# Performance work log

Measured on AMD Instinct MI355X. Metric: run time of the kernel, lower is better.

Reference implementation:

```python
import jax, jax.numpy as jnp
import numpy as np


def setup_inputs() -> dict:
    key = jax.random.key(0)
    k1, k2 = jax.random.split(key)
    B, C, H, W_ = 16, 512, 64, 64
    x = jax.random.normal(k1, (B, C, H, W_), dtype=jnp.float32)
    W = jax.random.normal(k2, (C, C), dtype=jnp.float32) * (1.0 / np.sqrt(C))
    return {"x": x, "W": W}


def reference(x, W):
    B, C, H, Wd = x.shape
    hw = H * Wd
    x1 = x.reshape(B, C, hw)                      # [B, C, HW]
    # linearW applied to x1^T: [B, HW, C] @ W^T -> [B, HW, C]
    x1_corr = jnp.einsum('bch,dc->bhd', x1, W)    # [B, HW, C]
    s = jnp.einsum('bch,bhd->bcd', x1, x1_corr)   # [B, C, C]
    a = jax.nn.softmax(s, axis=2)
    a = jax.nn.softmax(a, axis=1)
    out = jnp.einsum('bcd,bdh->bch', a, x1) + x1  # [B, C, HW]
    return out.reshape(B, C, H, Wd)
```

## Files before the change

### kernel.cpp

```cpp
#include <hip/hip_runtime.h>


typedef __attribute__((ext_vector_type(8))) short bf16x8;
typedef __attribute__((ext_vector_type(4))) float f32x4;

#define DEVINL __device__ __forceinline__
#define CFENCE() asm volatile("" ::: "memory")

DEVINL unsigned short f2bf(float f) {
  union { float f; unsigned int u; } c; c.f = f;
  unsigned int u = c.u;
  u += 0x7fffu + ((u >> 16) & 1u);
  return (unsigned short)(u >> 16);
}

DEVINL float bf2f(unsigned short h) {
  union { unsigned int u; float f; } c; c.u = ((unsigned int)h) << 16;
  return c.f;
}

DEVINL void gld_lds16(const unsigned short* g, unsigned short* l) {
  __builtin_amdgcn_global_load_lds(
      (const __attribute__((address_space(1))) unsigned int*)g,
      (__attribute__((address_space(3))) unsigned int*)l,
      16 , 0, 0);
}

template<int N> DEVINL void vm_wait() {
  if constexpr (N == 0)       asm volatile("s_waitcnt vmcnt(0)" ::: "memory");
  else if constexpr (N == 2)  asm volatile("s_waitcnt vmcnt(2)" ::: "memory");
  else if constexpr (N == 4)  asm volatile("s_waitcnt vmcnt(4)" ::: "memory");
  else if constexpr (N == 6)  asm volatile("s_waitcnt vmcnt(6)" ::: "memory");
  else if constexpr (N == 8)  asm volatile("s_waitcnt vmcnt(8)" ::: "memory");
  else if constexpr (N == 12) asm volatile("s_waitcnt vmcnt(12)" ::: "memory");
  else static_assert(N < 0, "unsupported vmcnt");
}

DEVINL void sym_tile_decode(int t, int& tm, int& tn) {
  if (t < 4)      { tm = 0; tn = t; }
  else if (t < 7) { tm = 1; tn = t - 3; }
  else if (t < 9) { tm = 2; tn = t - 5; }
  else            { tm = 3; tn = 3; }
}

__global__ __launch_bounds__(256)
void cvt_kernel(const float* __restrict__ in, unsigned short* __restrict__ out, int n4) {
  int i = blockIdx.x * 256 + threadIdx.x;
  const int stride = gridDim.x * 256;
  for (; i < n4; i += stride) {
    float4 v = ((const float4*)in)[i];
    unsigned int lo = (unsigned int)f2bf(v.x) | ((unsigned int)f2bf(v.y) << 16);
    unsigned int hi = (unsigned int)f2bf(v.z) | ((unsigned int)f2bf(v.w) << 16);
    uint2 o; o.x = lo; o.y = hi;
    ((uint2*)out)[i] = o;
  }
}

__global__ __launch_bounds__(256)
void fused_cvt_transpose(const float* __restrict__ x, unsigned short* __restrict__ x_bf,
                         unsigned short* __restrict__ xT) {
  __shared__ unsigned int T[2][32][68];
  const int tid = threadIdx.x;
  const int b  = blockIdx.y;
  const int hs = blockIdx.x & 31;
  const int ct = blockIdx.x >> 5;
  const int h0 = hs * 128;
  const int hq = tid & 7;
  const int c2 = tid >> 3;

  uint4 pa[2], pb[2];
  long long rowA[2];
  #pragma unroll
  for (int hh = 0; hh < 2; ++hh) {
    const int hcol = h0 + hh * 64 + hq * 8;
    rowA[hh] = (long long)(b * 512 + ct * 64 + 2 * c2) * 4096 + hcol;
    float4 a0 = *(const float4*)(x + rowA[hh]);
    float4 a1 = *(const float4*)(x + rowA[hh] + 4);
    float4 b0 = *(const float4*)(x + rowA[hh] + 4096);
    float4 b1 = *(const float4*)(x + rowA[hh] + 4100);
    unsigned short ha[8], hb[8];
    ha[0]=f2bf(a0.x); ha[1]=f2bf(a0.y); ha[2]=f2bf(a0.z); ha[3]=f2bf(a0.w);
    ha[4]=f2bf(a1.x); ha[5]=f2bf(a1.y); ha[6]=f2bf(a1.z); ha[7]=f2bf(a1.w);
    hb[0]=f2bf(b0.x); hb[1]=f2bf(b0.y); hb[2]=f2bf(b0.z); hb[3]=f2bf(b0.w);
    hb[4]=f2bf(b1.x); hb[5]=f2bf(b1.y); hb[6]=f2bf(b1.z); hb[7]=f2bf(b1.w);
    pa[hh].x = (unsigned int)ha[0] | ((unsigned int)ha[1] << 16);
    pa[hh].y = (unsigned int)ha[2] | ((unsigned int)ha[3] << 16);
    pa[hh].z = (unsigned int)ha[4] | ((unsigned int)ha[5] << 16);
    pa[hh].w = (unsigned int)ha[6] | ((unsigned int)ha[7] << 16);
    pb[hh].x = (unsigned int)hb[0] | ((unsigned int)hb[1] << 16);
    pb[hh].y = (unsigned int)hb[2] | ((unsigned int)hb[3] << 16);
    pb[hh].z = (unsigned int)hb[4] | ((unsigned int)hb[5] << 16);
    pb[hh].w = (unsigned int)hb[6] | ((unsigned int)hb[7] << 16);
    uint4 u0, u1;
    u0.x = (unsigned int)ha[0] | ((unsigned int)hb[0] << 16);
    u0.y = (unsigned int)ha[1] | ((unsigned int)hb[1] << 16);
    u0.z = (unsigned int)ha[2] | ((unsigned int)hb[2] << 16);
    u0.w = (unsigned int)ha[3] | ((unsigned int)hb[3] << 16);
    u1.x = (unsigned int)ha[4] | ((unsigned int)hb[4] << 16);
    u1.y = (unsigned int)ha[5] | ((unsigned int)hb[5] << 16);
    u1.z = (unsigned int)ha[6] | ((unsigned int)hb[6] << 16);
    u1.w = (unsigned int)ha[7] | ((unsigned int)hb[7] << 16);
    *(uint4*)&T[hh][c2][hq * 8]     = u0;
    *(uint4*)&T[hh][c2][hq * 8 + 4] = u1;
  }
  asm volatile("s_waitcnt lgkmcnt(0)" ::: "memory");
  __builtin_amdgcn_s_barrier();
  #pragma unroll
  for (int hh = 0; hh < 2; ++hh) {
    *(uint4*)(x_bf + rowA[hh])        = pa[hh];
    *(uint4*)(x_bf + rowA[hh] + 4096) = pb[hh];
  }
  const int h = tid >> 2, seg = tid & 3;
  #pragma unroll
  for (int hh = 0; hh < 2; ++hh) {
    unsigned int uu[8];
    #pragma unroll
    for (int i = 0; i < 8; ++i) uu[i] = T[hh][seg * 8 + i][h];
    unsigned int* dst = (unsigned int*)(xT +
        ((long long)(b * 4096 + h0 + hh * 64 + h) * 512 + ct * 64 + seg * 16));
    uint4 o0, o1;
    o0.x = uu[0]; o0.y = uu[1]; o0.z = uu[2]; o0.w = uu[3];
    o1.x = uu[4]; o1.y = uu[5]; o1.z = uu[6]; o1.w = uu[7];
    *(uint4*)dst = o0;
    *((uint4*)dst + 1) = o1;
  }
}

__global__ __launch_bounds__(256)
void gemm_gsym(const unsigned short* __restrict__ X, float* __restrict__ P) {
  constexpr int HALF = 128 * 32;
  __shared__ unsigned short As[3 * HALF];
  __shared__ unsigned short Bs[3 * HALF];
  const int tid = threadIdx.x;
  const int l   = tid & 63;
  const int w   = tid >> 6;
  const int wr  = w >> 1, wc = w & 1;
  const int b   = blockIdx.y;
  const int t   = blockIdx.x >> 2;
  const int split = blockIdx.x & 3;
  int tm, tn; sym_tile_decode(t, tm, tn);

  const unsigned short* Ab = X + (long long)b * 2097152 + (long long)(tm * 128) * 4096;
  const unsigned short* Bb = X + (long long)b * 2097152 + (long long)(tn * 128) * 4096;

  f32x4 acc[4][4];
  #pragma unroll
  for (int m = 0; m < 4; ++m)
    #pragma unroll
    for (int n = 0; n < 4; ++n) acc[m][n] = (f32x4){0.f, 0.f, 0.f, 0.f};

  const int srow = tid >> 2;
  const int scol = ((tid & 3) ^ ((tid >> 3) & 3)) * 8;
  const int ch8  = (((l >> 4) ^ ((l >> 1) & 3)) * 8);

  auto stage = [&](int buf, int k0) {
    #pragma unroll
    for (int i = 0; i < 2; ++i)
      gld_lds16(Ab + (long long)(i * 64 + srow) * 4096 + k0 + scol, &As[buf * HALF + i * 2048 + tid * 8]);
    #pragma unroll
    for (int i = 0; i < 2; ++i)
      gld_lds16(Bb + (long long)(i * 64 + srow) * 4096 + k0 + scol, &Bs[buf * HALF + i * 2048 + tid * 8]);
  };
  auto compute = [&](int buf) {
    bf16x8 af[4], bfr[4];
    #pragma unroll
    for (int m = 0; m < 4; ++m)
      af[m] = *(const bf16x8*)&As[buf * HALF + (wr * 64 + m * 16 + (l & 15)) * 32 + ch8];
    #pragma unroll
    for (int n = 0; n < 4; ++n)
      bfr[n] = *(const bf16x8*)&Bs[buf * HALF + (wc * 64 + n * 16 + (l & 15)) * 32 + ch8];
    __builtin_amdgcn_s_setprio(1);
    #pragma unroll
    for (int m = 0; m < 4; ++m)
      #pragma unroll
      for (int n = 0; n < 4; ++n)
        acc[m][n] = __builtin_amdgcn_mfma_f32_16x16x32_bf16(af[m], bfr[n], acc[m][n], 0, 0, 0);
    __builtin_amdgcn_s_setprio(0);
  };

  const int k_beg = split * 1024;
  constexpr int NK = 32;
  stage(0, k_beg);
  stage(1, k_beg + 32);
  int cb = 0, sbuf = 2, ks = k_beg + 64;
  for (int k = 0; k < NK - 2; ++k) {
    stage(sbuf, ks);
    ks += 32;
    sbuf = (sbuf == 2) ? 0 : sbuf + 1;
    vm_wait<8>();
    CFENCE(); __builtin_amdgcn_s_barrier(); CFENCE();
    compute(cb);
    CFENCE(); __builtin_amdgcn_s_barrier(); CFENCE();
    cb = (cb == 2) ? 0 : cb + 1;
  }
  vm_wait<4>();
  CFENCE(); __builtin_amdgcn_s_barrier(); CFENCE();
  compute(cb);
  cb = (cb == 2) ? 0 : cb + 1;
  vm_wait<0>();
  CFENCE(); __builtin_amdgcn_s_barrier(); CFENCE();
  compute(cb);

  float* Pt = P + (((long long)b * 10 + t) * 4 + split) * 16384;
  const int cc = l & 15, r4 = (l >> 4) * 4;
  #pragma unroll
  for (int m = 0; m < 4; ++m) {
    #pragma unroll
    for (int n = 0; n < 4; ++n) {
      const int row = wr * 64 + m * 16 + r4;
      const int col = wc * 64 + n * 16 + cc;
      #pragma unroll
      for (int j = 0; j < 4; ++j)
        Pt[(row + j) * 128 + col] = acc[m][n][j];
    }
  }
}

__global__ __launch_bounds__(256)
void reduce_mirror(const float* __restrict__ P, unsigned short* __restrict__ G) {
  __shared__ unsigned short T[128 * 129];
  const int tid = threadIdx.x;
  const int b = blockIdx.y;
  const int t = blockIdx.x;
  int tm, tn; sym_tile_decode(t, tm, tn);
  const float* Pt = P + ((long long)(b * 10 + t) * 4) * 16384;
  unsigned short* Gb = G + (long long)b * 262144;

  #pragma unroll
  for (int e = 0; e < 16; ++e) {
    const int v = e * 256 + tid;
    float4 s0 = ((const float4*)Pt)[v];
    float4 s1 = ((const float4*)(Pt + 16384))[v];
    float4 s2 = ((const float4*)(Pt + 32768))[v];
    float4 s3 = ((const float4*)(Pt + 49152))[v];
    unsigned int h0 = f2bf(s0.x + s1.x + s2.x + s3.x);
    unsigned int h1 = f2bf(s0.y + s1.y + s2.y + s3.y);
    unsigned int h2 = f2bf(s0.z + s1.z + s2.z + s3.z);
    unsigned int h3 = f2bf(s0.w + s1.w + s2.w + s3.w);
    const int idx = v * 4;
    const int r = idx >> 7, c = idx & 127;
    unsigned int* gp = (unsigned int*)(Gb + (long long)(tm * 128 + r) * 512 + tn * 128 + c);
    gp[0] = h0 | (h1 << 16);
    gp[1] = h2 | (h3 << 16);
    unsigned short* tp = &T[r * 129 + c];
    tp[0] = (unsigned short)h0; tp[1] = (unsigned short)h1;
    tp[2] = (unsigned short)h2; tp[3] = (unsigned short)h3;
  }
  if (tm != tn) {
    __syncthreads();
    #pragma unroll
    for (int e = 0; e < 16; ++e) {
      const int idx = (e * 256 + tid) * 4;
      const int r = idx >> 7, c = idx & 127;
      unsigned int o0 = T[(c + 0) * 129 + r], o1 = T[(c + 1) * 129 + r];
      unsigned int o2 = T[(c + 2) * 129 + r], o3 = T[(c + 3) * 129 + r];
      unsigned int* gp = (unsigned int*)(Gb + (long long)(tn * 128 + r) * 512 + tm * 128 + c);
      gp[0] = o0 | (o1 << 16);
      gp[1] = o2 | (o3 << 16);
    }
  }
}

__global__ __launch_bounds__(256)
void gemm_s(const unsigned short* __restrict__ A, const unsigned short* __restrict__ B,
            float* __restrict__ C) {
  constexpr int HALF = 64 * 32;
  __shared__ unsigned short As[3 * HALF];
  __shared__ unsigned short Bs[3 * HALF];

  const int tid = threadIdx.x;
  const int l   = tid & 63;
  const int w   = tid >> 6;
  const int wr  = w >> 1, wc = w & 1;
  const int bz  = blockIdx.y;
  const int tm  = blockIdx.x >> 3;
  const int tn  = blockIdx.x & 7;

  const unsigned short* Ab = A + (long long)bz * 262144 + (long long)(tm * 64) * 512;
  const unsigned short* Bb = B + (long long)(tn * 64) * 512;

  f32x4 acc[2][2];
  #pragma unroll
  for (int m = 0; m < 2; ++m)
    #pragma unroll
    for (int n = 0; n < 2; ++n) acc[m][n] = (f32x4){0.f, 0.f, 0.f, 0.f};

  const int srow = tid >> 2;
  const int scol = ((tid & 3) ^ ((tid >> 3) & 3)) * 8;
  const int ch8  = (((l >> 4) ^ ((l >> 1) & 3)) * 8);

  auto stage = [&](int buf, int k0) {
    gld_lds16(Ab + (long long)srow * 512 + k0 + scol, &As[buf * HALF + tid * 8]);
    gld_lds16(Bb + (long long)srow * 512 + k0 + scol, &Bs[buf * HALF + tid * 8]);
  };
  auto compute = [&](int buf) {
    bf16x8 af[2], bfr[2];
    #pragma unroll
    for (int m = 0; m < 2; ++m)
      af[m] = *(const bf16x8*)&As[buf * HALF + (wr * 32 + m * 16 + (l & 15)) * 32 + ch8];
    #pragma unroll
    for (int n = 0; n < 2; ++n)
      bfr[n] = *(const bf16x8*)&Bs[buf * HALF + (wc * 32 + n * 16 + (l & 15)) * 32 + ch8];
    __builtin_amdgcn_s_setprio(1);
    #pragma unroll
    for (int m = 0; m < 2; ++m)
      #pragma unroll
      for (int n = 0; n < 2; ++n)
        acc[m][n] = __builtin_amdgcn_mfma_f32_16x16x32_bf16(af[m], bfr[n], acc[m][n], 0, 0, 0);
    __builtin_amdgcn_s_setprio(0);
  };

  stage(0, 0);
  stage(1, 32);
  int cb = 0, sbuf = 2, ks = 64;
  for (int k = 0; k < 14; ++k) {
    stage(sbuf, ks);
    ks += 32;
    sbuf = (sbuf == 2) ? 0 : sbuf + 1;
    vm_wait<4>();
    CFENCE(); __builtin_amdgcn_s_barrier(); CFENCE();
    compute(cb);
    CFENCE(); __builtin_amdgcn_s_barrier(); CFENCE();
    cb = (cb == 2) ? 0 : cb + 1;
  }
  vm_wait<2>();
  CFENCE(); __builtin_amdgcn_s_barrier(); CFENCE();
  compute(cb);
  cb = (cb == 2) ? 0 : cb + 1;
  vm_wait<0>();
  CFENCE(); __builtin_amdgcn_s_barrier(); CFENCE();
  compute(cb);

  const int cc = l & 15, r4 = (l >> 4) * 4;
  const int row0 = tm * 64 + wr * 32;
  const int col0 = tn * 64 + wc * 32;
  #pragma unroll
  for (int m = 0; m < 2; ++m) {
    #pragma unroll
    for (int n = 0; n < 2; ++n) {
      const int row = row0 + m * 16 + r4;
      const int col = col0 + n * 16 + cc;
      long long base = (long long)bz * 262144 + (long long)row * 512 + col;
      #pragma unroll
      for (int j = 0; j < 4; ++j)
        C[base + (long long)j * 512] = acc[m][n][j];
    }
  }
}

__global__ __launch_bounds__(256)
void gemm_out(const unsigned short* __restrict__ A, const unsigned short* __restrict__ B,
              float* __restrict__ C) {
  constexpr int HALF_A = 128 * 32;
  constexpr int HALF_B = 256 * 32;
  __shared__ unsigned short As[3 * HALF_A];
  __shared__ unsigned short Bs[3 * HALF_B];

  const int tid = threadIdx.x;
  const int l   = tid & 63;
  const int w   = tid >> 6;
  const int bz  = blockIdx.y;
  const int tm  = blockIdx.x >> 4;
  const int tn  = blockIdx.x & 15;

  const unsigned short* Ab = A + (long long)bz * 262144  + (long long)(tm * 128) * 512;
  const unsigned short* Bb = B + (long long)bz * 2097152 + (long long)(tn * 256) * 512;

  f32x4 acc[8][4];
  #pragma unroll
  for (int m = 0; m < 8; ++m)
    #pragma unroll
    for (int n = 0; n < 4; ++n) acc[m][n] = (f32x4){0.f, 0.f, 0.f, 0.f};

  const int srow = tid >> 2;
  const int scol = ((tid & 3) ^ ((tid >> 3) & 3)) * 8;
  const int ch8  = (((l >> 4) ^ ((l >> 1) & 3)) * 8);

  auto stage = [&](int buf, int k0) {
    #pragma unroll
    for (int i = 0; i < 2; ++i)
      gld_lds16(Ab + (long long)(i * 64 + srow) * 512 + k0 + scol, &As[buf * HALF_A + i * 2048 + tid * 8]);
    #pragma unroll
    for (int i = 0; i < 4; ++i)
      gld_lds16(Bb + (long long)(i * 64 + srow) * 512 + k0 + scol, &Bs[buf * HALF_B + i * 2048 + tid * 8]);
  };
  auto compute = [&](int buf) {
    bf16x8 af[8], bfr[4];
    #pragma unroll
    for (int m = 0; m < 8; ++m)
      af[m] = *(const bf16x8*)&As[buf * HALF_A + (m * 16 + (l & 15)) * 32 + ch8];
    #pragma unroll
    for (int n = 0; n < 4; ++n)
      bfr[n] = *(const bf16x8*)&Bs[buf * HALF_B + (w * 64 + n * 16 + (l & 15)) * 32 + ch8];
    __builtin_amdgcn_s_setprio(1);
    #pragma unroll
    for (int m = 0; m < 8; ++m)
      #pragma unroll
      for (int n = 0; n < 4; ++n)
        acc[m][n] = __builtin_amdgcn_mfma_f32_16x16x32_bf16(af[m], bfr[n], acc[m][n], 0, 0, 0);
    __builtin_amdgcn_s_setprio(0);
  };

  stage(0, 0);
  stage(1, 32);
  int cb = 0, sbuf = 2, ks = 64;
  for (int k = 0; k < 14; ++k) {
    stage(sbuf, ks);
    ks += 32;
    sbuf = (sbuf == 2) ? 0 : sbuf + 1;
    vm_wait<12>();
    CFENCE(); __builtin_amdgcn_s_barrier(); CFENCE();
    compute(cb);
    CFENCE(); __builtin_amdgcn_s_barrier(); CFENCE();
    cb = (cb == 2) ? 0 : cb + 1;
  }
  vm_wait<6>();
  CFENCE(); __builtin_amdgcn_s_barrier(); CFENCE();
  compute(cb);
  cb = (cb == 2) ? 0 : cb + 1;
  vm_wait<0>();
  CFENCE(); __builtin_amdgcn_s_barrier(); CFENCE();
  compute(cb);

  const int cc = l & 15, r4 = (l >> 4) * 4;
  const int row0 = tm * 128;
  const int col0 = tn * 256 + w * 64;
  #pragma unroll
  for (int m = 0; m < 8; ++m) {
    #pragma unroll
    for (int n = 0; n < 4; ++n) {
      const int row = row0 + m * 16 + r4;
      const int col = col0 + n * 16 + cc;
      long long base = (long long)bz * 2097152 + (long long)row * 4096 + col;
      #pragma unroll
      for (int j = 0; j < 4; ++j)
        C[base + (long long)j * 4096] = acc[m][n][j];
    }
  }
}

__global__ __launch_bounds__(256)
void row_softmax_kernel(const float* __restrict__ s, unsigned short* __restrict__ p_bf) {
  __shared__ float red[4], red2[4];
  const float* p = s + (long long)blockIdx.x * 512;
  unsigned short* q = p_bf + (long long)blockIdx.x * 512;
  const int tid = threadIdx.x;
  float v0 = p[tid], v1 = p[tid + 256];
  float m = fmaxf(v0, v1);
  #pragma unroll
  for (int i = 1; i < 64; i <<= 1) m = fmaxf(m, __shfl_xor(m, i));
  if ((tid & 63) == 0) red[tid >> 6] = m;
  __syncthreads();
  m = fmaxf(fmaxf(red[0], red[1]), fmaxf(red[2], red[3]));
  float e0 = __expf(v0 - m), e1 = __expf(v1 - m);
  float sum = e0 + e1;
  #pragma unroll
  for (int i = 1; i < 64; i <<= 1) sum += __shfl_xor(sum, i);
  if ((tid & 63) == 0) red2[tid >> 6] = sum;
  __syncthreads();
  sum = (red2[0] + red2[1]) + (red2[2] + red2[3]);
  float inv = 1.0f / sum;
  q[tid] = f2bf(e0 * inv);
  q[tid + 256] = f2bf(e1 * inv);
}

__global__ __launch_bounds__(256)
void col_softmax_kernel(const unsigned short* __restrict__ p_bf, unsigned short* __restrict__ a_bf) {
  __shared__ float cs[8][32];
  const int tid = threadIdx.x;
  const int dl = tid & 31;
  const int st = tid >> 5;
  const int d  = blockIdx.x * 32 + dl;
  const long long base = (long long)blockIdx.y * 262144 + d;
  const unsigned short* p = p_bf + base;
  float sum = 0.f;
  #pragma unroll 4
  for (int c = st * 64; c < st * 64 + 64; ++c)
    sum += __expf(bf2f(p[(long long)c * 512]));
  cs[st][dl] = sum;
  __syncthreads();
  if (st == 0) {
    float s = ((cs[0][dl] + cs[1][dl]) + (cs[2][dl] + cs[3][dl]))
            + ((cs[4][dl] + cs[5][dl]) + (cs[6][dl] + cs[7][dl]));
    cs[0][dl] = 1.0f / s;
  }
  __syncthreads();
  const float inv = cs[0][dl];
  unsigned short* q = a_bf + base;
  #pragma unroll 4
  for (int c = st * 64; c < st * 64 + 64; ++c) {
    float v = __expf(bf2f(p[(long long)c * 512])) * inv;
    if (c == d) v += 1.0f;
    q[(long long)c * 512] = f2bf(v);
  }
}

extern "C" void kernel_launch(void* const* d_in, const int* in_sizes, int n_in,
                              void* d_out, int out_size, void* d_ws, size_t ws_size,
                              hipStream_t stream) {
  (void)in_sizes; (void)n_in; (void)out_size; (void)ws_size;
  const float* x = (const float*)d_in[0];
  const float* W = (const float*)d_in[1];
  float* out = (float*)d_out;
  char* ws = (char*)d_ws;

  unsigned short* x_bf = (unsigned short*)d_out;
  float* P = (float*)((char*)d_out + 67108864);
  unsigned short* p_bf = (unsigned short*)((char*)d_out + 67108864);

  unsigned short* xT   = (unsigned short*)ws;
  unsigned short* G_bf = (unsigned short*)(ws + 67108864);
  float*          s_f  = (float*)(ws + 75497472);
  unsigned short* W_bf = (unsigned short*)(ws + 92274688);
  unsigned short* a_bf = G_bf;

  fused_cvt_transpose<<<dim3(256, 16), 256, 0, stream>>>(x, x_bf, xT);
  cvt_kernel<<<256, 256, 0, stream>>>(W, W_bf, 65536);

  gemm_gsym<<<dim3(40, 16), 256, 0, stream>>>(x_bf, P);

  reduce_mirror<<<dim3(10, 16), 256, 0, stream>>>(P, G_bf);

  gemm_s<<<dim3(64, 16), 256, 0, stream>>>(G_bf, W_bf, s_f);

  row_softmax_kernel<<<8192, 256, 0, stream>>>(s_f, p_bf);
  col_softmax_kernel<<<dim3(16, 16), 256, 0, stream>>>(p_bf, a_bf);

  gemm_out<<<dim3(64, 16), 256, 0, stream>>>(a_bf, xT, out);
}
```

Measured before the change: 189.0 us.

## Drop xT transpose, transpose X in gemm_out LDS, bf16 split-K partials

Removes the fused convert+transpose kernel and its extra write of a transposed bf16 copy of x. gemm_out now reads row-major x_bf directly, interleaving pairs of rows in registers before writing them to padded LDS, with a new double-buffered pipeline and a 128x128 tile on twice as many blocks. The split-K partials from gemm_gsym are stored as bf16 instead of fp32, halving that traffic at some precision cost. Pipelines in gemm_gsym and gemm_s drop from triple to double buffering, and output stores become nontemporal.

```diff
diff --git a/kernel.cpp b/kernel.cpp
--- a/kernel.cpp
+++ b/kernel.cpp
@@ -32,9 +32,10 @@
   else if constexpr (N == 4)  asm volatile("s_waitcnt vmcnt(4)" ::: "memory");
   else if constexpr (N == 6)  asm volatile("s_waitcnt vmcnt(6)" ::: "memory");
   else if constexpr (N == 8)  asm volatile("s_waitcnt vmcnt(8)" ::: "memory");
-  else if constexpr (N == 12) asm volatile("s_waitcnt vmcnt(12)" ::: "memory");
   else static_assert(N < 0, "unsupported vmcnt");
 }
+
+DEVINL void lgkm0() { asm volatile("s_waitcnt lgkmcnt(0)" ::: "memory"); }
 
 DEVINL void sym_tile_decode(int t, int& tm, int& tn) {
   if (t < 4)      { tm = 0; tn = t; }
@@ -57,80 +58,10 @@
 }
 
 __global__ __launch_bounds__(256)
-void fused_cvt_transpose(const float* __restrict__ x, unsigned short* __restrict__ x_bf,
-                         unsigned short* __restrict__ xT) {
-  __shared__ unsigned int T[2][32][68];
-  const int tid = threadIdx.x;
-  const int b  = blockIdx.y;
-  const int hs = blockIdx.x & 31;
-  const int ct = blockIdx.x >> 5;
-  const int h0 = hs * 128;
-  const int hq = tid & 7;
-  const int c2 = tid >> 3;
-
-  uint4 pa[2], pb[2];
-  long long rowA[2];
-  #pragma unroll
-  for (int hh = 0; hh < 2; ++hh) {
-    const int hcol = h0 + hh * 64 + hq * 8;
-    rowA[hh] = (long long)(b * 512 + ct * 64 + 2 * c2) * 4096 + hcol;
-    float4 a0 = *(const float4*)(x + rowA[hh]);
-    float4 a1 = *(const float4*)(x + rowA[hh] + 4);
-    float4 b0 = *(const float4*)(x + rowA[hh] + 4096);
-    float4 b1 = *(const float4*)(x + rowA[hh] + 4100);
-    unsigned short ha[8], hb[8];
-    ha[0]=f2bf(a0.x); ha[1]=f2bf(a0.y); ha[2]=f2bf(a0.z); ha[3]=f2bf(a0.w);
-    ha[4]=f2bf(a1.x); ha[5]=f2bf(a1.y); ha[6]=f2bf(a1.z); ha[7]=f2bf(a1.w);
-    hb[0]=f2bf(b0.x); hb[1]=f2bf(b0.y); hb[2]=f2bf(b0.z); hb[3]=f2bf(b0.w);
-    hb[4]=f2bf(b1.x); hb[5]=f2bf(b1.y); hb[6]=f2bf(b1.z); hb[7]=f2bf(b1.w);
-    pa[hh].x = (unsigned int)ha[0] | ((unsigned int)ha[1] << 16);
-    pa[hh].y = (unsigned int)ha[2] | ((unsigned int)ha[3] << 16);
-    pa[hh].z = (unsigned int)ha[4] | ((unsigned int)ha[5] << 16);
-    pa[hh].w = (unsigned int)ha[6] | ((unsigned int)ha[7] << 16);
-    pb[hh].x = (unsigned int)hb[0] | ((unsigned int)hb[1] << 16);
-    pb[hh].y = (unsigned int)hb[2] | ((unsigned int)hb[3] << 16);
-    pb[hh].z = (unsigned int)hb[4] | ((unsigned int)hb[5] << 16);
-    pb[hh].w = (unsigned int)hb[6] | ((unsigned int)hb[7] << 16);
-    uint4 u0, u1;
-    u0.x = (unsigned int)ha[0] | ((unsigned int)hb[0] << 16);
-    u0.y = (unsigned int)ha[1] | ((unsigned int)hb[1] << 16);
-    u0.z = (unsigned int)ha[2] | ((unsigned int)hb[2] << 16);
-    u0.w = (unsigned int)ha[3] | ((unsigned int)hb[3] << 16);
-    u1.x = (unsigned int)ha[4] | ((unsigned int)hb[4] << 16);
-    u1.y = (unsigned int)ha[5] | ((unsigned int)hb[5] << 16);
-    u1.z = (unsigned int)ha[6] | ((unsigned int)hb[6] << 16);
-    u1.w = (unsigned int)ha[7] | ((unsigned int)hb[7] << 16);
-    *(uint4*)&T[hh][c2][hq * 8]     = u0;
-    *(uint4*)&T[hh][c2][hq * 8 + 4] = u1;
-  }
-  asm volatile("s_waitcnt lgkmcnt(0)" ::: "memory");
-  __builtin_amdgcn_s_barrier();
-  #pragma unroll
-  for (int hh = 0; hh < 2; ++hh) {
-    *(uint4*)(x_bf + rowA[hh])        = pa[hh];
-    *(uint4*)(x_bf + rowA[hh] + 4096) = pb[hh];
-  }
-  const int h = tid >> 2, seg = tid & 3;
-  #pragma unroll
-  for (int hh = 0; hh < 2; ++hh) {
-    unsigned int uu[8];
-    #pragma unroll
-    for (int i = 0; i < 8; ++i) uu[i] = T[hh][seg * 8 + i][h];
-    unsigned int* dst = (unsigned int*)(xT +
-        ((long long)(b * 4096 + h0 + hh * 64 + h) * 512 + ct * 64 + seg * 16));
-    uint4 o0, o1;
-    o0.x = uu[0]; o0.y = uu[1]; o0.z = uu[2]; o0.w = uu[3];
-    o1.x = uu[4]; o1.y = uu[5]; o1.z = uu[6]; o1.w = uu[7];
-    *(uint4*)dst = o0;
-    *((uint4*)dst + 1) = o1;
-  }
-}
-
-__global__ __launch_bounds__(256)
-void gemm_gsym(const unsigned short* __restrict__ X, float* __restrict__ P) {
+void gemm_gsym(const unsigned short* __restrict__ X, unsigned short* __restrict__ P) {
   constexpr int HALF = 128 * 32;
-  __shared__ unsigned short As[3 * HALF];
-  __shared__ unsigned short Bs[3 * HALF];
+  __shared__ unsigned short As[2 * HALF];
+  __shared__ unsigned short Bs[2 * HALF];
   const int tid = threadIdx.x;
   const int l   = tid & 63;
   const int w   = tid >> 6;
@@ -182,26 +113,22 @@
   constexpr int NK = 32;
   stage(0, k_beg);
   stage(1, k_beg + 32);
-  int cb = 0, sbuf = 2, ks = k_beg + 64;
+  int ks = k_beg + 64;
   for (int k = 0; k < NK - 2; ++k) {
-    stage(sbuf, ks);
-    ks += 32;
-    sbuf = (sbuf == 2) ? 0 : sbuf + 1;
-    vm_wait<8>();
-    CFENCE(); __builtin_amdgcn_s_barrier(); CFENCE();
-    compute(cb);
-    CFENCE(); __builtin_amdgcn_s_barrier(); CFENCE();
-    cb = (cb == 2) ? 0 : cb + 1;
+    vm_wait<4>();
+    CFENCE(); __builtin_amdgcn_s_barrier(); CFENCE();
+    compute(k & 1);
+    CFENCE(); __builtin_amdgcn_s_barrier(); CFENCE();
+    stage(k & 1, ks); ks += 32;
   }
   vm_wait<4>();
   CFENCE(); __builtin_amdgcn_s_barrier(); CFENCE();
-  compute(cb);
-  cb = (cb == 2) ? 0 : cb + 1;
+  compute((NK - 2) & 1);
   vm_wait<0>();
   CFENCE(); __builtin_amdgcn_s_barrier(); CFENCE();
-  compute(cb);
-
-  float* Pt = P + (((long long)b * 10 + t) * 4 + split) * 16384;
+  compute((NK - 1) & 1);
+
+  unsigned short* Pt = P + (((long long)b * 10 + t) * 4 + split) * 16384;
   const int cc = l & 15, r4 = (l >> 4) * 4;
   #pragma unroll
   for (int m = 0; m < 4; ++m) {
@@ -211,32 +138,32 @@
       const int col = wc * 64 + n * 16 + cc;
       #pragma unroll
       for (int j = 0; j < 4; ++j)
-        Pt[(row + j) * 128 + col] = acc[m][n][j];
+        Pt[(row + j) * 128 + col] = f2bf(acc[m][n][j]);
     }
   }
 }
 
 __global__ __launch_bounds__(256)
-void reduce_mirror(const float* __restrict__ P, unsigned short* __restrict__ G) {
+void reduce_mirror(const unsigned short* __restrict__ P, unsigned short* __restrict__ G) {
   __shared__ unsigned short T[128 * 129];
   const int tid = threadIdx.x;
   const int b = blockIdx.y;
   const int t = blockIdx.x;
   int tm, tn; sym_tile_decode(t, tm, tn);
-  const float* Pt = P + ((long long)(b * 10 + t) * 4) * 16384;
+  const unsigned short* Pt = P + ((long long)(b * 10 + t) * 4) * 16384;
   unsigned short* Gb = G + (long long)b * 262144;
 
   #pragma unroll
   for (int e = 0; e < 16; ++e) {
     const int v = e * 256 + tid;
-    float4 s0 = ((const float4*)Pt)[v];
-    float4 s1 = ((const float4*)(Pt + 16384))[v];
-    float4 s2 = ((const float4*)(Pt + 32768))[v];
-    float4 s3 = ((const float4*)(Pt + 49152))[v];
-    unsigned int h0 = f2bf(s0.x + s1.x + s2.x + s3.x);
-    unsigned int h1 = f2bf(s0.y + s1.y + s2.y + s3.y);
-    unsigned int h2 = f2bf(s0.z + s1.z + s2.z + s3.z);
-    unsigned int h3 = f2bf(s0.w + s1.w + s2.w + s3.w);
+    ushort4 s0 = ((const ushort4*)Pt)[v];
+    ushort4 s1 = ((const ushort4*)(Pt + 16384))[v];
+    ushort4 s2 = ((const ushort4*)(Pt + 32768))[v];
+    ushort4 s3 = ((const ushort4*)(Pt + 49152))[v];
+    unsigned int h0 = f2bf(bf2f(s0.x) + bf2f(s1.x) + bf2f(s2.x) + bf2f(s3.x));
+    unsigned int h1 = f2bf(bf2f(s0.y) + bf2f(s1.y) + bf2f(s2.y) + bf2f(s3.y));
+    unsigned int h2 = f2bf(bf2f(s0.z) + bf2f(s1.z) + bf2f(s2.z) + bf2f(s3.z));
+    unsigned int h3 = f2bf(bf2f(s0.w) + bf2f(s1.w) + bf2f(s2.w) + bf2f(s3.w));
     const int idx = v * 4;
     const int r = idx >> 7, c = idx & 127;
     unsigned int* gp = (unsigned int*)(Gb + (long long)(tm * 128 + r) * 512 + tn * 128 + c);
@@ -265,8 +192,8 @@
 void gemm_s(const unsigned short* __restrict__ A, const unsigned short* __restrict__ B,
             float* __restrict__ C) {
   constexpr int HALF = 64 * 32;
-  __shared__ unsigned short As[3 * HALF];
-  __shared__ unsigned short Bs[3 * HALF];
+  __shared__ unsigned short As[2 * HALF];
+  __shared__ unsigned short Bs[2 * HALF];
 
   const int tid = threadIdx.x;
   const int l   = tid & 63;
@@ -312,24 +239,20 @@
 
   stage(0, 0);
   stage(1, 32);
-  int cb = 0, sbuf = 2, ks = 64;
+  int ks = 64;
   for (int k = 0; k < 14; ++k) {
-    stage(sbuf, ks);
-    ks += 32;
-    sbuf = (sbuf == 2) ? 0 : sbuf + 1;
-    vm_wait<4>();
-    CFENCE(); __builtin_amdgcn_s_barrier(); CFENCE();
-    compute(cb);
-    CFENCE(); __builtin_amdgcn_s_barrier(); CFENCE();
-    cb = (cb == 2) ? 0 : cb + 1;
+    vm_wait<2>();
+    CFENCE(); __builtin_amdgcn_s_barrier(); CFENCE();
+    compute(k & 1);
+    CFENCE(); __builtin_amdgcn_s_barrier(); CFENCE();
+    stage(k & 1, ks); ks += 32;
   }
   vm_wait<2>();
   CFENCE(); __builtin_amdgcn_s_barrier(); CFENCE();
-  compute(cb);
-  cb = (cb == 2) ? 0 : cb + 1;
+  compute(0);
   vm_wait<0>();
   CFENCE(); __builtin_amdgcn_s_barrier(); CFENCE();
-  compute(cb);
+  compute(1);
 
   const int cc = l & 15, r4 = (l >> 4) * 4;
   const int row0 = tm * 64 + wr * 32;
@@ -349,84 +272,125 @@
 }
 
 __global__ __launch_bounds__(256)
-void gemm_out(const unsigned short* __restrict__ A, const unsigned short* __restrict__ B,
+void gemm_out(const unsigned short* __restrict__ A, const unsigned short* __restrict__ X,
               float* __restrict__ C) {
-  constexpr int HALF_A = 128 * 32;
-  constexpr int HALF_B = 256 * 32;
-  __shared__ unsigned short As[3 * HALF_A];
-  __shared__ unsigned short Bs[3 * HALF_B];
+  __shared__ unsigned short As[2][128 * 32];
+  __shared__ unsigned int   Bs[2][16][132];
 
   const int tid = threadIdx.x;
   const int l   = tid & 63;
   const int w   = tid >> 6;
+  const int wr  = w >> 1, wc = w & 1;
   const int bz  = blockIdx.y;
-  const int tm  = blockIdx.x >> 4;
-  const int tn  = blockIdx.x & 15;
+  const int tm  = blockIdx.x >> 5;
+  const int tn  = blockIdx.x & 31;
 
   const unsigned short* Ab = A + (long long)bz * 262144  + (long long)(tm * 128) * 512;
-  const unsigned short* Bb = B + (long long)bz * 2097152 + (long long)(tn * 256) * 512;
-
-  f32x4 acc[8][4];
-  #pragma unroll
-  for (int m = 0; m < 8; ++m)
+  const unsigned short* Xb = X + (long long)bz * 2097152 + tn * 128;
+
+  f32x4 acc[4][4];
+  #pragma unroll
+  for (int m = 0; m < 4; ++m)
     #pragma unroll
     for (int n = 0; n < 4; ++n) acc[m][n] = (f32x4){0.f, 0.f, 0.f, 0.f};
 
   const int srow = tid >> 2;
   const int scol = ((tid & 3) ^ ((tid >> 3) & 3)) * 8;
   const int ch8  = (((l >> 4) ^ ((l >> 1) & 3)) * 8);
-
-  auto stage = [&](int buf, int k0) {
+  const int bp_  = tid >> 4;
+  const int bh_  = tid & 15;
+  const unsigned short* Bsrc = Xb + (long long)(2 * bp_) * 4096 + bh_ * 8;
+
+  auto Agload = [&](int buf, int k0) {
     #pragma unroll
     for (int i = 0; i < 2; ++i)
-      gld_lds16(Ab + (long long)(i * 64 + srow) * 512 + k0 + scol, &As[buf * HALF_A + i * 2048 + tid * 8]);
-    #pragma unroll
-    for (int i = 0; i < 4; ++i)
-      gld_lds16(Bb + (long long)(i * 64 + srow) * 512 + k0 + scol, &Bs[buf * HALF_B + i * 2048 + tid * 8]);
+      gld_lds16(Ab + (long long)(i * 64 + srow) * 512 + k0 + scol, &As[buf][i * 2048 + tid * 8]);
+  };
+  auto Bload = [&](int k0, uint4& g0, uint4& g1) {
+    g0 = *(const uint4*)(Bsrc + (long long)k0 * 4096);
+    g1 = *(const uint4*)(Bsrc + (long long)(k0 + 1) * 4096);
+  };
+  auto Bdswrite = [&](int buf, const uint4& g0, const uint4& g1) {
+    unsigned int w0 = (g0.x & 0xffffu) | (g1.x << 16);
+    unsigned int w1 = (g0.x >> 16)    | (g1.x & 0xffff0000u);
+    unsigned int w2 = (g0.y & 0xffffu) | (g1.y << 16);
+    unsigned int w3 = (g0.y >> 16)    | (g1.y & 0xffff0000u);
+    unsigned int w4 = (g0.z & 0xffffu) | (g1.z << 16);
+    unsigned int w5 = (g0.z >> 16)    | (g1.z & 0xffff0000u);
+    unsigned int w6 = (g0.w & 0xffffu) | (g1.w << 16);
+    unsigned int w7 = (g0.w >> 16)    | (g1.w & 0xffff0000u);
+    unsigned int* dst = &Bs[buf][bp_][bh_ * 8];
+    uint4 o0; o0.x = w0; o0.y = w1; o0.z = w2; o0.w = w3;
+    uint4 o1; o1.x = w4; o1.y = w5; o1.z = w6; o1.w = w7;
+    *(uint4*)dst = o0;
+    *(uint4*)(dst + 4) = o1;
   };
   auto compute = [&](int buf) {
-    bf16x8 af[8], bfr[4];
-    #pragma unroll
-    for (int m = 0; m < 8; ++m)
-      af[m] = *(const bf16x8*)&As[buf * HALF_A + (m * 16 + (l & 15)) * 32 + ch8];
-    #pragma unroll
-    for (int n = 0; n < 4; ++n)
-      bfr[n] = *(const bf16x8*)&Bs[buf * HALF_B + (w * 64 + n * 16 + (l & 15)) * 32 + ch8];
+    bf16x8 af[4], bfr[4];
+    #pragma unroll
+    for (int m = 0; m < 4; ++m)
+      af[m] = *(const bf16x8*)&As[buf][(wr * 64 + m * 16 + (l & 15)) * 32 + ch8];
+    const int hl = wc * 64 + (l & 15);
+    const int p0 = (l >> 4) * 4;
+    #pragma unroll
+    for (int n = 0; n < 4; ++n) {
+      unsigned int wv[4];
+      #pragma unroll
+      for (int i = 0; i < 4; ++i) wv[i] = Bs[buf][p0 + i][hl + n * 16];
+      bfr[n] = *(bf16x8*)wv;
+    }
     __builtin_amdgcn_s_setprio(1);
     #pragma unroll
-    for (int m = 0; m < 8; ++m)
+    for (int m = 0; m < 4; ++m)
       #pragma unroll
       for (int n = 0; n < 4; ++n)
         acc[m][n] = __builtin_amdgcn_mfma_f32_16x16x32_bf16(af[m], bfr[n], acc[m][n], 0, 0, 0);
     __builtin_amdgcn_s_setprio(0);
   };
 
-  stage(0, 0);
-  stage(1, 32);
-  int cb = 0, sbuf = 2, ks = 64;
-  for (int k = 0; k < 14; ++k) {
-    stage(sbuf, ks);
-    ks += 32;
-    sbuf = (sbuf == 2) ? 0 : sbuf + 1;
-    vm_wait<12>();
-    CFENCE(); __builtin_amdgcn_s_barrier(); CFENCE();
-    compute(cb);
-    CFENCE(); __builtin_amdgcn_s_barrier(); CFENCE();
-    cb = (cb == 2) ? 0 : cb + 1;
-  }
+  uint4 e0, e1, o0, o1;
+  Bload(0, e0, e1);
+  Agload(0, 0);
+  Bload(32, o0, o1);
+  Agload(1, 32);
   vm_wait<6>();
-  CFENCE(); __builtin_amdgcn_s_barrier(); CFENCE();
-  compute(cb);
-  cb = (cb == 2) ? 0 : cb + 1;
+  Bdswrite(0, e0, e1);
+  lgkm0();
+  CFENCE(); __builtin_amdgcn_s_barrier(); CFENCE();
+
+  #pragma unroll 1
+  for (int kk = 0; kk < 7; ++kk) {
+    const int k = 2 * kk;
+    vm_wait<4>();
+    compute(0);
+    vm_wait<2>();
+    Bdswrite(1, o0, o1);
+    lgkm0();
+    CFENCE(); __builtin_amdgcn_s_barrier(); CFENCE();
+    Bload((k + 2) * 32, e0, e1);
+    Agload(0, (k + 2) * 32);
+    vm_wait<4>();
+    compute(1);
+    vm_wait<2>();
+    Bdswrite(0, e0, e1);
+    lgkm0();
+    CFENCE(); __builtin_amdgcn_s_barrier(); CFENCE();
+    Bload((k + 3) * 32, o0, o1);
+    Agload(1, (k + 3) * 32);
+  }
+  vm_wait<4>();
+  compute(0);
   vm_wait<0>();
-  CFENCE(); __builtin_amdgcn_s_barrier(); CFENCE();
-  compute(cb);
+  Bdswrite(1, o0, o1);
+  lgkm0();
+  CFENCE(); __builtin_amdgcn_s_barrier(); CFENCE();
+  compute(1);
 
   const int cc = l & 15, r4 = (l >> 4) * 4;
-  const int row0 = tm * 128;
-  const int col0 = tn * 256 + w * 64;
-  #pragma unroll
-  for (int m = 0; m < 8; ++m) {
+  const int row0 = tm * 128 + wr * 64;
+  const int col0 = tn * 128 + wc * 64;
+  #pragma unroll
+  for (int m = 0; m < 4; ++m) {
     #pragma unroll
     for (int n = 0; n < 4; ++n) {
       const int row = row0 + m * 16 + r4;
@@ -434,7 +398,7 @@
       long long base = (long long)bz * 2097152 + (long long)row * 4096 + col;
       #pragma unroll
       for (int j = 0; j < 4; ++j)
-        C[base + (long long)j * 4096] = acc[m][n][j];
+        __builtin_nontemporal_store(acc[m][n][j], &C[base + (long long)j * 4096]);
     }
   }
 }
@@ -504,17 +468,16 @@
   float* out = (float*)d_out;
   char* ws = (char*)d_ws;
 
-  unsigned short* x_bf = (unsigned short*)d_out;
-  float* P = (float*)((char*)d_out + 67108864);
-  unsigned short* p_bf = (unsigned short*)((char*)d_out + 67108864);
-
-  unsigned short* xT   = (unsigned short*)ws;
+  unsigned short* P    = (unsigned short*)((char*)d_out + 67108864);
+  unsigned short* p_bf = (unsigned short*)((char*)d_out + 88080384);
+
+  unsigned short* x_bf = (unsigned short*)ws;
   unsigned short* G_bf = (unsigned short*)(ws + 67108864);
   float*          s_f  = (float*)(ws + 75497472);
   unsigned short* W_bf = (unsigned short*)(ws + 92274688);
   unsigned short* a_bf = G_bf;
 
-  fused_cvt_transpose<<<dim3(256, 16), 256, 0, stream>>>(x, x_bf, xT);
+  cvt_kernel<<<4096, 256, 0, stream>>>(x, x_bf, 8388608);
   cvt_kernel<<<256, 256, 0, stream>>>(W, W_bf, 65536);
 
   gemm_gsym<<<dim3(40, 16), 256, 0, stream>>>(x_bf, P);
@@ -526,5 +489,5 @@
   row_softmax_kernel<<<8192, 256, 0, stream>>>(s_f, p_bf);
   col_softmax_kernel<<<dim3(16, 16), 256, 0, stream>>>(p_bf, a_bf);
 
-  gemm_out<<<dim3(64, 16), 256, 0, stream>>>(a_bf, xT, out);
-}
+  gemm_out<<<dim3(128, 16), 256, 0, stream>>>(a_bf, x_bf, out);
+}
```

New measurement: 164.9 us. -12.7%, faster.
